# Kernel optimization log

Measured on AMD Instinct MI355X. Metric: run time of the kernel, lower is better.

Reference implementation:

```python
import jax, jax.numpy as jnp
import numpy as np

A, B, D, H, O = 64, 4096, 50, 192, 3

def _xavier(key, shape, gain=0.5):
    fan_in, fan_out = shape[-1], shape[-2]
    limit = gain * np.sqrt(6.0 / (fan_in + fan_out))
    return jax.random.uniform(key, shape, jnp.float32, -limit, limit)

def setup_inputs() -> dict:
    key = jax.random.key(0)
    ks = jax.random.split(key, 12)
    return {
        "x": jax.random.normal(ks[0], (B, D), jnp.float32),
        "input_norm_weight": _xavier(ks[1], (A, D)),
        "input_norm_bias": jnp.zeros((A, D), jnp.float32),
        "layer1_weight": _xavier(ks[2], (A, H, D)),
        "layer1_bias": jnp.zeros((A, H), jnp.float32),
        "layer2_weight": _xavier(ks[3], (A, H, H)),
        "layer2_bias": jnp.zeros((A, H), jnp.float32),
        "layer3_weight": _xavier(ks[4], (A, H, H)),
        "layer3_bias": jnp.zeros((A, H), jnp.float32),
        "output_weight": _xavier(ks[5], (A, O, H)),
        "output_bias": jnp.zeros((A, O), jnp.float32),
        "skip1_weight": _xavier(ks[6], (A, H, D)),
        "skip1_bias": jnp.zeros((A, H), jnp.float32),
        "skip2_weight": _xavier(ks[7], (A, H, H)),
        "skip2_bias": jnp.zeros((A, H), jnp.float32),
        "hidden_norm_weight": _xavier(ks[8], (A, H)),
        "hidden_norm_bias": jnp.zeros((A, H), jnp.float32),
    }

def reference(x, input_norm_weight, input_norm_bias,
              layer1_weight, layer1_bias, layer2_weight, layer2_bias,
              layer3_weight, layer3_bias, output_weight, output_bias,
              skip1_weight, skip1_bias, skip2_weight, skip2_bias,
              hidden_norm_weight, hidden_norm_bias):
    # NOTE: the vectorized ensemble's "norms" are affine-only (no mean/var), per source.
    # x: [B, D] -> broadcast over agents: [A, B, D]
    x_norm = x[None, :, :] * input_norm_weight[:, None, :] + input_norm_bias[:, None, :]
    gelu = lambda t: jax.nn.gelu(t, approximate=False)  # torch F.gelu exact
    # per-agent GEMMs: [A,B,in] x [A,out,in] -> [A,B,out]
    h1 = gelu(jnp.einsum('abi,ahi->abh', x_norm, layer1_weight) + layer1_bias[:, None, :]) \
         + jnp.einsum('abi,ahi->abh', x_norm, skip1_weight) + skip1_bias[:, None, :]
    h2 = gelu(jnp.einsum('abi,ahi->abh', h1, layer2_weight) + layer2_bias[:, None, :]) \
         + jnp.einsum('abi,ahi->abh', h1, skip2_weight) + skip2_bias[:, None, :]
    h3 = jnp.einsum('abi,ahi->abh', h2, layer3_weight) + layer3_bias[:, None, :] + h2
    h3 = h3 * hidden_norm_weight[:, None, :] + hidden_norm_bias[:, None, :]
    logits = jnp.einsum('abh,aoh->abo', h3, output_weight) + output_bias[:, None, :]
    return logits  # [A, B, O]
```

## Files before the change

kernel.cpp:

```cpp
#include <hip/hip_runtime.h>
#include <math.h>

#define A_N 64
#define B_N 4096
#define D_N 50
#define H_N 192
#define O_N 3

typedef __attribute__((ext_vector_type(8))) __bf16 bf16x8;
typedef __attribute__((ext_vector_type(4))) __bf16 bf16x4;
typedef __attribute__((ext_vector_type(4))) float f32x4;

#define W1_OFF   0
#define S1_OFF   786432
#define W2_OFF   1572864
#define S2_OFF   3932160
#define W3_OFF   6291456
#define OW_OFF   8650752
#define WS_ELEMS 8847360

#if __has_builtin(__builtin_amdgcn_rcpf)
#define FRCP(x) __builtin_amdgcn_rcpf(x)
#else
#define FRCP(x) (1.0f / (x))
#endif
#if __has_builtin(__builtin_amdgcn_exp2f)
#define FEXP2(x) __builtin_amdgcn_exp2f(x)
#else
#define FEXP2(x) exp2f(x)
#endif

__device__ __forceinline__ float gelu_f(float xx) {
    float t  = 0.70710678118654752440f * xx;
    float at = fabsf(t);
    float k  = FRCP(fmaf(0.3275911f, at, 1.0f));
    float p  = fmaf(k, 1.061405429f, -1.453152027f);
    p = fmaf(k, p, 1.421413741f);
    p = fmaf(k, p, -0.284496736f);
    p = fmaf(k, p, 0.254829592f);
    p = p * k;
    float e  = FEXP2(t * t * -1.44269504088896340736f);
    float er = fmaf(-p, e, 1.0f);
    er = (t < 0.f) ? -er : er;
    return 0.5f * xx * (1.0f + er);
}

__global__ __launch_bounds__(256)
void prep_kernel(const float* __restrict__ w1, const float* __restrict__ s1,
                 const float* __restrict__ w2, const float* __restrict__ s2,
                 const float* __restrict__ w3, const float* __restrict__ ow,
                 __bf16* __restrict__ ws) {
    __shared__ __bf16 T[192 * 72];
    const int b   = blockIdx.x;
    const int tid = threadIdx.x;

    if (b < 1152) {
        int m  = b / 384;
        int r  = b % 384;
        int a  = r / 6;
        int rc = r % 6;
        const float* src = ((m == 0) ? w2 : (m == 1) ? s2 : w3) + (size_t)a * 36864;
        __bf16* dst = ws + ((m == 0) ? W2_OFF : (m == 1) ? S2_OFF : W3_OFF) + (size_t)a * 36864;
        #pragma unroll
        for (int i = 0; i < 6; ++i) {
            int f4 = i * 256 + tid;
            int row = f4 / 48, kc = (f4 % 48) * 4;
            f32x4 v = *(const f32x4*)(src + (size_t)(rc * 32 + row) * 192 + kc);
            bf16x4 o;
            #pragma unroll
            for (int j = 0; j < 4; ++j) o[j] = (__bf16)v[j];
            *(bf16x4*)(T + row * 200 + kc) = o;
        }
        __syncthreads();
        #pragma unroll
        for (int i = 0; i < 3; ++i) {
            int fr = i * 256 + tid;
            int f = fr >> 6, lane = fr & 63;
            int ntl = f / 6, ks = f % 6;
            int n = ntl * 16 + (lane & 15), k = ks * 32 + (lane >> 4) * 8;
            bf16x8 v = *(const bf16x8*)(T + n * 200 + k);
            *(bf16x8*)(dst + ((size_t)(rc * 2 + ntl) * 6 + ks) * 512 + lane * 8) = v;
        }
    } else if (b < 1280) {
        int r = b - 1152; int m = r >> 6; int a = r & 63;
        const float* src = (m ? s1 : w1) + (size_t)a * 9600;
        __bf16* dst = ws + (m ? S1_OFF : W1_OFF) + (size_t)a * 12288;
        for (int e = tid; e < 192 * 72; e += 256) T[e] = (__bf16)0.f;
        __syncthreads();
        for (int e = tid; e < 9600; e += 256) {
            int row = e / 50, k = e - row * 50;
            T[row * 72 + k] = (__bf16)src[e];
        }
        __syncthreads();
        #pragma unroll
        for (int i = 0; i < 6; ++i) {
            int fr = i * 256 + tid;
            int f = fr >> 6, lane = fr & 63;
            int nt = f >> 1, ks = f & 1;
            int n = nt * 16 + (lane & 15), k = ks * 32 + (lane >> 4) * 8;
            bf16x8 v = *(const bf16x8*)(T + n * 72 + k);
            *(bf16x8*)(dst + (size_t)(nt * 2 + ks) * 512 + lane * 8) = v;
        }
    } else {
        int r = b - 1280;
        #pragma unroll
        for (int i = 0; i < 8; ++i) {
            int fr = (r * 8 + i) * 256 + tid;
            int a = fr / 384, rem = fr - a * 384;
            int ks = rem >> 6, lane = rem & 63;
            int n = lane & 15, k = ks * 32 + (lane >> 4) * 8;
            bf16x8 v;
            if (n < O_N) {
                const float* p = ow + ((size_t)a * O_N + n) * H_N + k;
                f32x4 f0 = *(const f32x4*)p, f1 = *(const f32x4*)(p + 4);
                #pragma unroll
                for (int j = 0; j < 4; ++j) { v[j] = (__bf16)f0[j]; v[4 + j] = (__bf16)f1[j]; }
            } else {
                #pragma unroll
                for (int j = 0; j < 8; ++j) v[j] = (__bf16)0.f;
            }
            *(bf16x8*)(ws + OW_OFF + (size_t)a * 3072 + ks * 512 + lane * 8) = v;
        }
    }
}

#define MFMA(a, b, c) __builtin_amdgcn_mfma_f32_16x16x32_bf16((a), (b), (c), 0, 0, 0)

__global__ __launch_bounds__(256, 3)
void srek_mfma(const float* __restrict__ x,
               const float* __restrict__ inw, const float* __restrict__ inb,
               const float* __restrict__ b1,  const float* __restrict__ b2,
               const float* __restrict__ b3,  const float* __restrict__ s1b,
               const float* __restrict__ s2b, const float* __restrict__ hnw,
               const float* __restrict__ hnb, const float* __restrict__ ob,
               const __bf16* __restrict__ ws, float* __restrict__ out) {
    __shared__ __bf16 Xs[8 * 512];
    __shared__ __bf16 Hs[24 * 512];

    const int bid  = blockIdx.x;
    const int slot = bid >> 3;
    const int tile = slot & 63;
    const int a    = ((bid & 7) << 3) | (slot >> 6);
    const int row0 = tile * 64;

    const int tid  = threadIdx.x;
    const int lane = tid & 63;
    const int wv   = tid >> 6;
    const int ln   = lane & 15;
    const int quad = lane >> 4;
    const int aH   = a * H_N;
    const int c0   = wv * 48;
    const int l8   = lane * 8;
    const int f3   = wv * 3;

    const __bf16* W1 = ws + W1_OFF + (size_t)a * 12288;
    const __bf16* S1 = ws + S1_OFF + (size_t)a * 12288;
    const __bf16* W2 = ws + W2_OFF + (size_t)a * 36864;
    const __bf16* S2 = ws + S2_OFF + (size_t)a * 36864;
    const __bf16* W3 = ws + W3_OFF + (size_t)a * 36864;
    const __bf16* OWp= ws + OW_OFF + (size_t)a * 3072;

    bf16x8 nxt[6];
    f32x4 accT[12], accS[12], h2f[12];
    const f32x4 zero = {0.f, 0.f, 0.f, 0.f};

    #pragma unroll
    for (int t = 0; t < 3; ++t) {
        nxt[t]     = *(const bf16x8*)(W1 + ((f3 + t) * 2 + 0) * 512 + l8);
        nxt[3 + t] = *(const bf16x8*)(S1 + ((f3 + t) * 2 + 0) * 512 + l8);
    }

    for (int e = tid; e < 8 * 512; e += 256) {
        int j   = e & 7;
        int lnn = (e >> 3) & 15;
        int qd  = (e >> 7) & 3;
        int kss = (e >> 9) & 1;
        int mtt = (e >> 10) & 3;
        int r = mtt * 16 + lnn;
        int k = kss * 32 + qd * 8 + j;
        float v = 0.f;
        if (k < D_N) v = x[(size_t)(row0 + r) * D_N + k] * inw[a * D_N + k] + inb[a * D_N + k];
        Xs[e] = (__bf16)v;
    }

    auto compute_dual = [&](const __bf16* As, int KS, int ks,
                            const bf16x8* cw, const bf16x8* cs) {
        #pragma unroll
        for (int mt = 0; mt < 4; ++mt) {
            bf16x8 av = *(const bf16x8*)(As + (mt * KS + ks) * 512 + l8);
            #pragma unroll
            for (int t = 0; t < 3; ++t) {
                accT[mt * 3 + t] = MFMA(cw[t], av, accT[mt * 3 + t]);
                accS[mt * 3 + t] = MFMA(cs[t], av, accS[mt * 3 + t]);
            }
        }
    };
    auto compute_single = [&](int ks, const bf16x8* cw) {
        #pragma unroll
        for (int mt = 0; mt < 4; ++mt) {
            bf16x8 av = *(const bf16x8*)(Hs + (mt * 6 + ks) * 512 + l8);
            #pragma unroll
            for (int t = 0; t < 3; ++t)
                accT[mt * 3 + t] = MFMA(cw[t], av, accT[mt * 3 + t]);
        }
    };
    auto store_fragmajor = [&](const f32x4* src) {
        #pragma unroll
        for (int t = 0; t < 3; ++t) {
            int ks2 = (3 * wv + t) >> 1;
            int qp  = (6 * wv + 2 * t + (quad >> 1)) & 3;
            int off = (qp * 16 + ln) * 8 + (quad & 1) * 4;
            #pragma unroll
            for (int mt = 0; mt < 4; ++mt) {
                bf16x4 o;
                #pragma unroll
                for (int rg = 0; rg < 4; ++rg) o[rg] = (__bf16)src[mt * 3 + t][rg];
                *(bf16x4*)(Hs + (mt * 6 + ks2) * 512 + off) = o;
            }
        }
    };

    #pragma unroll
    for (int i = 0; i < 12; ++i) { accT[i] = zero; accS[i] = zero; }
    __syncthreads();

    {
        bf16x8 cw[3], cs[3];
        #pragma unroll
        for (int t = 0; t < 3; ++t) { cw[t] = nxt[t]; cs[t] = nxt[3 + t]; }
        #pragma unroll
        for (int t = 0; t < 3; ++t) {
            nxt[t]     = *(const bf16x8*)(W1 + ((f3 + t) * 2 + 1) * 512 + l8);
            nxt[3 + t] = *(const bf16x8*)(S1 + ((f3 + t) * 2 + 1) * 512 + l8);
        }
        compute_dual(Xs, 2, 0, cw, cs);
        #pragma unroll
        for (int t = 0; t < 3; ++t) { cw[t] = nxt[t]; cs[t] = nxt[3 + t]; }
        #pragma unroll
        for (int t = 0; t < 3; ++t) {
            nxt[t]     = *(const bf16x8*)(W2 + ((f3 + t) * 6 + 0) * 512 + l8);
            nxt[3 + t] = *(const bf16x8*)(S2 + ((f3 + t) * 6 + 0) * 512 + l8);
        }
        compute_dual(Xs, 2, 1, cw, cs);
    }
    #pragma unroll
    for (int t = 0; t < 3; ++t) {
        int colb = c0 + t * 16 + quad * 4;
        f32x4 bb = *(const f32x4*)(b1 + aH + colb);
        f32x4 sb = *(const f32x4*)(s1b + aH + colb);
        #pragma unroll
        for (int mt = 0; mt < 4; ++mt)
            #pragma unroll
            for (int rg = 0; rg < 4; ++rg)
                h2f[mt * 3 + t][rg] = gelu_f(accT[mt * 3 + t][rg] + bb[rg]) + accS[mt * 3 + t][rg] + sb[rg];
    }
    store_fragmajor(h2f);
    #pragma unroll
    for (int i = 0; i < 12; ++i) { accT[i] = zero; accS[i] = zero; }
    __syncthreads();

    #pragma unroll
    for (int ks = 0; ks < 6; ++ks) {
        bf16x8 cw[3], cs[3];
        #pragma unroll
        for (int t = 0; t < 3; ++t) { cw[t] = nxt[t]; cs[t] = nxt[3 + t]; }
        if (ks < 5) {
            #pragma unroll
            for (int t = 0; t < 3; ++t) {
                nxt[t]     = *(const bf16x8*)(W2 + ((f3 + t) * 6 + ks + 1) * 512 + l8);
                nxt[3 + t] = *(const bf16x8*)(S2 + ((f3 + t) * 6 + ks + 1) * 512 + l8);
            }
        } else {
            #pragma unroll
            for (int t = 0; t < 3; ++t)
                nxt[t] = *(const bf16x8*)(W3 + ((f3 + t) * 6 + 0) * 512 + l8);
        }
        compute_dual(Hs, 6, ks, cw, cs);
    }
    #pragma unroll
    for (int t = 0; t < 3; ++t) {
        int colb = c0 + t * 16 + quad * 4;
        f32x4 bb = *(const f32x4*)(b2 + aH + colb);
        f32x4 sb = *(const f32x4*)(s2b + aH + colb);
        #pragma unroll
        for (int mt = 0; mt < 4; ++mt)
            #pragma unroll
            for (int rg = 0; rg < 4; ++rg)
                h2f[mt * 3 + t][rg] = gelu_f(accT[mt * 3 + t][rg] + bb[rg]) + accS[mt * 3 + t][rg] + sb[rg];
    }
    #pragma unroll
    for (int i = 0; i < 12; ++i) accT[i] = zero;
    __syncthreads();
    store_fragmajor(h2f);
    __syncthreads();

    bf16x8 ow6[6];
    #pragma unroll
    for (int ks = 0; ks < 6; ++ks) {
        bf16x8 cw[3];
        #pragma unroll
        for (int t = 0; t < 3; ++t) cw[t] = nxt[t];
        if (ks < 5) {
            #pragma unroll
            for (int t = 0; t < 3; ++t)
                nxt[t] = *(const bf16x8*)(W3 + ((f3 + t) * 6 + ks + 1) * 512 + l8);
        } else {
            #pragma unroll
            for (int kk = 0; kk < 6; ++kk)
                ow6[kk] = *(const bf16x8*)(OWp + kk * 512 + l8);
        }
        compute_single(ks, cw);
    }
    #pragma unroll
    for (int t = 0; t < 3; ++t) {
        int colb = c0 + t * 16 + quad * 4;
        f32x4 b3v = *(const f32x4*)(b3  + aH + colb);
        f32x4 nwv = *(const f32x4*)(hnw + aH + colb);
        f32x4 nbv = *(const f32x4*)(hnb + aH + colb);
        #pragma unroll
        for (int mt = 0; mt < 4; ++mt)
            #pragma unroll
            for (int rg = 0; rg < 4; ++rg)
                h2f[mt * 3 + t][rg] = fmaf(accT[mt * 3 + t][rg] + b3v[rg] + h2f[mt * 3 + t][rg],
                                           nwv[rg], nbv[rg]);
    }
    __syncthreads();
    store_fragmajor(h2f);
    __syncthreads();

    {
        f32x4 acco = zero;
        #pragma unroll
        for (int ks = 0; ks < 6; ++ks) {
            bf16x8 av = *(const bf16x8*)(Hs + (wv * 6 + ks) * 512 + l8);
            acco = MFMA(ow6[ks], av, acco);
        }
        if (quad == 0) {
            float* po = out + ((size_t)a * B_N + row0 + wv * 16 + ln) * O_N;
            po[0] = acco[0] + ob[a * O_N + 0];
            po[1] = acco[1] + ob[a * O_N + 1];
            po[2] = acco[2] + ob[a * O_N + 2];
        }
    }
}

extern "C" void kernel_launch(void* const* d_in, const int* in_sizes, int n_in,
                              void* d_out, int out_size, void* d_ws, size_t ws_size,
                              hipStream_t stream) {
    const float* x   = (const float*)d_in[0];
    const float* inw = (const float*)d_in[1];
    const float* inb = (const float*)d_in[2];
    const float* w1  = (const float*)d_in[3];
    const float* b1  = (const float*)d_in[4];
    const float* w2  = (const float*)d_in[5];
    const float* b2  = (const float*)d_in[6];
    const float* w3  = (const float*)d_in[7];
    const float* b3  = (const float*)d_in[8];
    const float* ow  = (const float*)d_in[9];
    const float* ob  = (const float*)d_in[10];
    const float* s1w = (const float*)d_in[11];
    const float* s1b = (const float*)d_in[12];
    const float* s2w = (const float*)d_in[13];
    const float* s2b = (const float*)d_in[14];
    const float* hnw = (const float*)d_in[15];
    const float* hnb = (const float*)d_in[16];

    __bf16* ws = (__bf16*)d_ws;

    prep_kernel<<<dim3(1292), dim3(256), 0, stream>>>(w1, s1w, w2, s2w, w3, ow, ws);

    srek_mfma<<<dim3(A_N * (B_N / 64)), dim3(256), 0, stream>>>(
        x, inw, inb, b1, b2, b3, s1b, s2b, hnw, hnb, ob, ws, (float*)d_out);
}
```

Baseline: 226.3 us.

## Drop h2f register array, double-buffer LDS and fold biases into accumulators

Removes the 12-entry h2f fp32 register array by writing activations straight to shared memory and seeding the accumulators with the biases, so the epilogues no longer add them. A second 24-fragment shared buffer (replacing the small input buffer) lets layer-2 output go to a different buffer from the one being read, which removes two __syncthreads. The residual h2 plus b3 is kept in accT as the initial value for the layer-3 MFMA. Packed bf16 conversion intrinsics are used for the stores. Together these aim to lower VGPR pressure and barrier count, at the cost of more LDS per block, which could limit occupancy.

```diff
diff --git a/kernel.cpp b/kernel.cpp
--- a/kernel.cpp
+++ b/kernel.cpp
@@ -1,4 +1,5 @@
 #include <hip/hip_runtime.h>
+#include <hip/hip_bf16.h>
 #include <math.h>
 
 #define A_N 64
@@ -45,6 +46,13 @@
     return 0.5f * xx * (1.0f + er);
 }
 
+__device__ __forceinline__ bf16x4 pk_bf16x4(const f32x4 v) {
+    union { bf16x4 v4; __hip_bfloat162 h2[2]; } u;
+    u.h2[0] = __float22bfloat162_rn(make_float2(v[0], v[1]));
+    u.h2[1] = __float22bfloat162_rn(make_float2(v[2], v[3]));
+    return u.v4;
+}
+
 __global__ __launch_bounds__(256)
 void prep_kernel(const float* __restrict__ w1, const float* __restrict__ s1,
                  const float* __restrict__ w2, const float* __restrict__ s2,
@@ -66,10 +74,7 @@
             int f4 = i * 256 + tid;
             int row = f4 / 48, kc = (f4 % 48) * 4;
             f32x4 v = *(const f32x4*)(src + (size_t)(rc * 32 + row) * 192 + kc);
-            bf16x4 o;
-            #pragma unroll
-            for (int j = 0; j < 4; ++j) o[j] = (__bf16)v[j];
-            *(bf16x4*)(T + row * 200 + kc) = o;
+            *(bf16x4*)(T + row * 200 + kc) = pk_bf16x4(v);
         }
         __syncthreads();
         #pragma unroll
@@ -134,7 +139,7 @@
                const float* __restrict__ s2b, const float* __restrict__ hnw,
                const float* __restrict__ hnb, const float* __restrict__ ob,
                const __bf16* __restrict__ ws, float* __restrict__ out) {
-    __shared__ __bf16 Xs[8 * 512];
+    __shared__ __bf16 Bu[24 * 512];
     __shared__ __bf16 Hs[24 * 512];
 
     const int bid  = blockIdx.x;
@@ -161,8 +166,7 @@
     const __bf16* OWp= ws + OW_OFF + (size_t)a * 3072;
 
     bf16x8 nxt[6];
-    f32x4 accT[12], accS[12], h2f[12];
-    const f32x4 zero = {0.f, 0.f, 0.f, 0.f};
+    f32x4 accT[12], accS[12];
 
     #pragma unroll
     for (int t = 0; t < 3; ++t) {
@@ -180,9 +184,19 @@
         int k = kss * 32 + qd * 8 + j;
         float v = 0.f;
         if (k < D_N) v = x[(size_t)(row0 + r) * D_N + k] * inw[a * D_N + k] + inb[a * D_N + k];
-        Xs[e] = (__bf16)v;
-    }
-
+        Bu[e] = (__bf16)v;
+    }
+
+    auto init_dual = [&](const float* bp, const float* sp) {
+        #pragma unroll
+        for (int t = 0; t < 3; ++t) {
+            int colb = c0 + t * 16 + quad * 4;
+            f32x4 bb = *(const f32x4*)(bp + aH + colb);
+            f32x4 sb = *(const f32x4*)(sp + aH + colb);
+            #pragma unroll
+            for (int mt = 0; mt < 4; ++mt) { accT[mt * 3 + t] = bb; accS[mt * 3 + t] = sb; }
+        }
+    };
     auto compute_dual = [&](const __bf16* As, int KS, int ks,
                             const bf16x8* cw, const bf16x8* cs) {
         #pragma unroll
@@ -195,33 +209,22 @@
             }
         }
     };
-    auto compute_single = [&](int ks, const bf16x8* cw) {
-        #pragma unroll
-        for (int mt = 0; mt < 4; ++mt) {
-            bf16x8 av = *(const bf16x8*)(Hs + (mt * 6 + ks) * 512 + l8);
+    auto compute_single = [&](const __bf16* As, int ks, const bf16x8* cw) {
+        #pragma unroll
+        for (int mt = 0; mt < 4; ++mt) {
+            bf16x8 av = *(const bf16x8*)(As + (mt * 6 + ks) * 512 + l8);
             #pragma unroll
             for (int t = 0; t < 3; ++t)
                 accT[mt * 3 + t] = MFMA(cw[t], av, accT[mt * 3 + t]);
         }
     };
-    auto store_fragmajor = [&](const f32x4* src) {
-        #pragma unroll
-        for (int t = 0; t < 3; ++t) {
-            int ks2 = (3 * wv + t) >> 1;
-            int qp  = (6 * wv + 2 * t + (quad >> 1)) & 3;
-            int off = (qp * 16 + ln) * 8 + (quad & 1) * 4;
-            #pragma unroll
-            for (int mt = 0; mt < 4; ++mt) {
-                bf16x4 o;
-                #pragma unroll
-                for (int rg = 0; rg < 4; ++rg) o[rg] = (__bf16)src[mt * 3 + t][rg];
-                *(bf16x4*)(Hs + (mt * 6 + ks2) * 512 + off) = o;
-            }
-        }
+    const int ks2_base = 3 * wv;
+    auto fm_off = [&](int t) {
+        int qp = (6 * wv + 2 * t + (quad >> 1)) & 3;
+        return (qp * 16 + ln) * 8 + (quad & 1) * 4;
     };
 
-    #pragma unroll
-    for (int i = 0; i < 12; ++i) { accT[i] = zero; accS[i] = zero; }
+    init_dual(b1, s1b);
     __syncthreads();
 
     {
@@ -233,7 +236,7 @@
             nxt[t]     = *(const bf16x8*)(W1 + ((f3 + t) * 2 + 1) * 512 + l8);
             nxt[3 + t] = *(const bf16x8*)(S1 + ((f3 + t) * 2 + 1) * 512 + l8);
         }
-        compute_dual(Xs, 2, 0, cw, cs);
+        compute_dual(Bu, 2, 0, cw, cs);
         #pragma unroll
         for (int t = 0; t < 3; ++t) { cw[t] = nxt[t]; cs[t] = nxt[3 + t]; }
         #pragma unroll
@@ -241,22 +244,21 @@
             nxt[t]     = *(const bf16x8*)(W2 + ((f3 + t) * 6 + 0) * 512 + l8);
             nxt[3 + t] = *(const bf16x8*)(S2 + ((f3 + t) * 6 + 0) * 512 + l8);
         }
-        compute_dual(Xs, 2, 1, cw, cs);
+        compute_dual(Bu, 2, 1, cw, cs);
     }
     #pragma unroll
     for (int t = 0; t < 3; ++t) {
-        int colb = c0 + t * 16 + quad * 4;
-        f32x4 bb = *(const f32x4*)(b1 + aH + colb);
-        f32x4 sb = *(const f32x4*)(s1b + aH + colb);
-        #pragma unroll
-        for (int mt = 0; mt < 4; ++mt)
+        int ks2 = (ks2_base + t) >> 1, off = fm_off(t);
+        #pragma unroll
+        for (int mt = 0; mt < 4; ++mt) {
+            f32x4 v;
             #pragma unroll
             for (int rg = 0; rg < 4; ++rg)
-                h2f[mt * 3 + t][rg] = gelu_f(accT[mt * 3 + t][rg] + bb[rg]) + accS[mt * 3 + t][rg] + sb[rg];
-    }
-    store_fragmajor(h2f);
-    #pragma unroll
-    for (int i = 0; i < 12; ++i) { accT[i] = zero; accS[i] = zero; }
+                v[rg] = gelu_f(accT[mt * 3 + t][rg]) + accS[mt * 3 + t][rg];
+            *(bf16x4*)(Hs + (mt * 6 + ks2) * 512 + off) = pk_bf16x4(v);
+        }
+    }
+    init_dual(b2, s2b);
     __syncthreads();
 
     #pragma unroll
@@ -279,19 +281,20 @@
     }
     #pragma unroll
     for (int t = 0; t < 3; ++t) {
+        int ks2 = (ks2_base + t) >> 1, off = fm_off(t);
         int colb = c0 + t * 16 + quad * 4;
-        f32x4 bb = *(const f32x4*)(b2 + aH + colb);
-        f32x4 sb = *(const f32x4*)(s2b + aH + colb);
-        #pragma unroll
-        for (int mt = 0; mt < 4; ++mt)
-            #pragma unroll
-            for (int rg = 0; rg < 4; ++rg)
-                h2f[mt * 3 + t][rg] = gelu_f(accT[mt * 3 + t][rg] + bb[rg]) + accS[mt * 3 + t][rg] + sb[rg];
-    }
-    #pragma unroll
-    for (int i = 0; i < 12; ++i) accT[i] = zero;
-    __syncthreads();
-    store_fragmajor(h2f);
+        f32x4 b3v = *(const f32x4*)(b3 + aH + colb);
+        #pragma unroll
+        for (int mt = 0; mt < 4; ++mt) {
+            f32x4 v;
+            #pragma unroll
+            for (int rg = 0; rg < 4; ++rg) {
+                v[rg] = gelu_f(accT[mt * 3 + t][rg]) + accS[mt * 3 + t][rg];
+                accT[mt * 3 + t][rg] = v[rg] + b3v[rg];
+            }
+            *(bf16x4*)(Bu + (mt * 6 + ks2) * 512 + off) = pk_bf16x4(v);
+        }
+    }
     __syncthreads();
 
     bf16x8 ow6[6];
@@ -309,27 +312,27 @@
             for (int kk = 0; kk < 6; ++kk)
                 ow6[kk] = *(const bf16x8*)(OWp + kk * 512 + l8);
         }
-        compute_single(ks, cw);
+        compute_single(Bu, ks, cw);
     }
     #pragma unroll
     for (int t = 0; t < 3; ++t) {
+        int ks2 = (ks2_base + t) >> 1, off = fm_off(t);
         int colb = c0 + t * 16 + quad * 4;
-        f32x4 b3v = *(const f32x4*)(b3  + aH + colb);
         f32x4 nwv = *(const f32x4*)(hnw + aH + colb);
         f32x4 nbv = *(const f32x4*)(hnb + aH + colb);
         #pragma unroll
-        for (int mt = 0; mt < 4; ++mt)
+        for (int mt = 0; mt < 4; ++mt) {
+            f32x4 v;
             #pragma unroll
             for (int rg = 0; rg < 4; ++rg)
-                h2f[mt * 3 + t][rg] = fmaf(accT[mt * 3 + t][rg] + b3v[rg] + h2f[mt * 3 + t][rg],
-                                           nwv[rg], nbv[rg]);
+                v[rg] = fmaf(accT[mt * 3 + t][rg], nwv[rg], nbv[rg]);
+            *(bf16x4*)(Hs + (mt * 6 + ks2) * 512 + off) = pk_bf16x4(v);
+        }
     }
     __syncthreads();
-    store_fragmajor(h2f);
-    __syncthreads();
 
     {
-        f32x4 acco = zero;
+        f32x4 acco = {0.f, 0.f, 0.f, 0.f};
         #pragma unroll
         for (int ks = 0; ks < 6; ++ks) {
             bf16x8 av = *(const bf16x8*)(Hs + (wv * 6 + ks) * 512 + l8);
```

Result: slower. 236.9 us (+4.7%).
